# Performance work log

Measured on AMD Instinct MI355X. Metric: run time of the kernel, lower is better.

## Reference

```python
import jax, jax.numpy as jnp
import numpy as np

N = 65536          # pixels
F = 224            # spectral bands (num_features)
P = 6              # num_endmembers
H = 256            # hidden_dim


def setup_inputs() -> dict:
    key = jax.random.key(0)
    ks = jax.random.split(key, 8)
    s = lambda fan_in: 1.0 / np.sqrt(fan_in)
    return {
        "abundance_matrix": jax.random.normal(ks[0], (N, P), jnp.float32),
        "Y": jax.random.normal(ks[1], (N, F), jnp.float32),
        "W1": jax.random.normal(ks[2], (F, H), jnp.float32) * s(F),
        "b1": jnp.zeros((H,), jnp.float32),
        "W2": jax.random.normal(ks[3], (H, H), jnp.float32) * s(H),
        "b2": jnp.zeros((H,), jnp.float32),
        "W3": jax.random.normal(ks[4], (H, F), jnp.float32) * s(H),
        "b3": jnp.zeros((F,), jnp.float32),
    }


def reference(abundance_matrix, Y, W1, b1, W2, b2, W3, b3):
    # MLP is pointwise over pixels, so apply once to all pixels [N,F] -> [N,F]
    h = jax.nn.relu(Y @ W1 + b1)
    h = jax.nn.relu(h @ W2 + b2)
    logits = h @ W3 + b3                      # [N, F]

    cls = jnp.argmax(abundance_matrix, axis=-1)          # [N]
    masks = cls[None, :] == jnp.arange(P)[:, None]       # [P, N]

    # Masked per-class softmax over the pixel axis (per feature column).
    neg = jnp.finfo(logits.dtype).min
    masked_logits = jnp.where(masks[:, :, None], logits[None], neg)  # [P, N, F]
    w = jax.nn.softmax(masked_logits, axis=1)                        # [P, N, F]
    w = w * masks[:, :, None]                                        # exact zeros off-class

    M = jnp.einsum('pnf,nf->pf', w, Y)                   # [P, F] endmembers
    counts = masks.sum(axis=1)                           # [P]
    M = jnp.where((counts > 0)[:, None], M, jnp.zeros_like(M))

    Y_hat = abundance_matrix @ M                         # [N, F]
    return Y_hat
```

## Files before the change

kernel.cpp:

```cpp
#include <hip/hip_runtime.h>
#include <stdint.h>

typedef short s16x8 __attribute__((ext_vector_type(8)));
typedef short s16x4 __attribute__((ext_vector_type(4)));
typedef float f32x4 __attribute__((ext_vector_type(4)));

#define NPIX 65536
#define FEAT 224
#define PEND 6
#define HID  256

__device__ __forceinline__ unsigned short f2bf(float x) {
  unsigned u = __float_as_uint(x);
  return (unsigned short)((u + 0x7FFFu + ((u >> 16) & 1u)) >> 16);
}
__device__ __forceinline__ float bf2f(unsigned short b) {
  return __uint_as_float(((unsigned)b) << 16);
}
__device__ __forceinline__ void glds16(const void* g, void* l) {
  __builtin_amdgcn_global_load_lds(
      (const __attribute__((address_space(1))) unsigned int*)g,
      (__attribute__((address_space(3))) unsigned int*)l, 16, 0, 0);
}

__global__ void cvtW_all(const float* __restrict__ W1, const float* __restrict__ W2,
                         const float* __restrict__ W3,
                         unsigned short* __restrict__ W1t, unsigned short* __restrict__ W2t,
                         unsigned short* __restrict__ W3t, float* __restrict__ gz) {
  int i = blockIdx.x * 256 + threadIdx.x;
  if (i < 57344) {
    int n = i / 224, k = i - n * 224;
    W1t[i] = f2bf(W1[k * 256 + n]);
  } else if (i < 122880) {
    int i2 = i - 57344;
    int n = i2 >> 8, k = i2 & 255;
    W2t[i2] = f2bf(W2[k * 256 + n]);
  } else if (i < 188416) {
    int i3 = i - 122880;
    int n = i3 >> 8, k = i3 & 255;
    W3t[i3] = (n < FEAT) ? f2bf(W3[k * FEAT + n]) : (unsigned short)0;
  } else if (i < 191104) {
    gz[i - 188416] = 0.f;
  }
}

__global__ __launch_bounds__(256, 2)
void fused_mlp(const float* __restrict__ Y,
               const unsigned short* __restrict__ W1t,
               const unsigned short* __restrict__ W2t,
               const unsigned short* __restrict__ W3t,
               const float* __restrict__ b1, const float* __restrict__ b2,
               const float* __restrict__ b3, const float* __restrict__ ab,
               float* __restrict__ gsum, float* __restrict__ gsumY) {
  __shared__ __align__(16) unsigned short hS[64 * 256];
  __shared__ __align__(16) unsigned short Bs[2][8192];
  unsigned short* AsB = hS;
  float* redE = (float*)&Bs[0][0];
  float* redY = redE + PEND * FEAT;
  unsigned short* clsS = (unsigned short*)(redY + PEND * FEAT);

  const int tid = threadIdx.x;
  const int wid = tid >> 6, lane = tid & 63;
  const int wm = wid >> 1, wn = wid & 1;
  const int mrow = lane & 15, quad = lane >> 4;
  const int brow = lane >> 2, bk8 = (lane & 3) * 8;
  const int arow = tid >> 2, aqtr = tid & 3;
  const long row0 = (long)blockIdx.x * 64;

  f32x4 acc[2][8];
  float4 pv0, pv1;

#define STAGE_W(s) do {                                                     \
    const unsigned short* Wp_; int ld_, k0_;                                \
    if ((s) < 7)       { Wp_ = W1t; ld_ = 224; k0_ = (s) * 32; }            \
    else if ((s) < 15) { Wp_ = W2t; ld_ = 256; k0_ = ((s) - 7) * 32; }      \
    else               { Wp_ = W3t; ld_ = 256; k0_ = ((s) - 15) * 32; }     \
    unsigned short* dst_ = &Bs[(s) & 1][wid * 2048];                        \
    _Pragma("unroll")                                                       \
    for (int c_ = 0; c_ < 4; c_++)                                          \
      glds16(Wp_ + (wid * 64 + c_ * 16 + brow) * ld_ + k0_ + bk8,           \
             dst_ + c_ * 512);                                              \
  } while (0)

#define LOADA(p) do {                                                       \
    const float* s_ = Y + (row0 + arow) * FEAT + (p) * 32 + aqtr * 8;       \
    pv0 = *(const float4*)s_; pv1 = *(const float4*)(s_ + 4);               \
  } while (0)

#define WRITEA(p) do {                                                      \
    unsigned short* d_ = AsB + ((p) & 1) * 2304 + arow * 36 + aqtr * 8;     \
    s16x4 lo_ = {(short)f2bf(pv0.x), (short)f2bf(pv0.y),                    \
                 (short)f2bf(pv0.z), (short)f2bf(pv0.w)};                   \
    s16x4 hi_ = {(short)f2bf(pv1.x), (short)f2bf(pv1.y),                    \
                 (short)f2bf(pv1.z), (short)f2bf(pv1.w)};                   \
    *(s16x4*)d_ = lo_; *(s16x4*)(d_ + 4) = hi_;                             \
  } while (0)

#define LOAD_B(buf)                                                         \
    _Pragma("unroll")                                                       \
    for (int j = 0; j < 8; j++)                                             \
      bfv[j] = *(const s16x8*)(&Bs[buf][(wn * 128 + j * 16 + mrow) * 32 + quad * 8]);

#define MFMA_ALL()                                                          \
    _Pragma("unroll")                                                       \
    for (int i = 0; i < 2; i++)                                             \
      _Pragma("unroll")                                                     \
      for (int j = 0; j < 8; j++)                                           \
        acc[i][j] = __builtin_amdgcn_mfma_f32_16x16x32_bf16(af[i], bfv[j], acc[i][j], 0, 0, 0);

#define ZERO_ACC()                                                          \
    _Pragma("unroll")                                                       \
    for (int i = 0; i < 2; i++)                                             \
      _Pragma("unroll")                                                     \
      for (int j = 0; j < 8; j++) acc[i][j] = {0.f, 0.f, 0.f, 0.f};

  ZERO_ACC();
  LOADA(0); STAGE_W(0); WRITEA(0);
  __syncthreads();
  for (int p = 0; p < 7; p++) {
    if (p < 6) { LOADA(p + 1); STAGE_W(p + 1); }
    else       { STAGE_W(7); }
    s16x8 af[2], bfv[8];
    const unsigned short* Ab = AsB + (p & 1) * 2304;
#pragma unroll
    for (int i = 0; i < 2; i++) {
      const unsigned short* pa = Ab + (wm * 32 + i * 16 + mrow) * 36 + quad * 8;
      s16x4 lo = *(const s16x4*)pa, hi = *(const s16x4*)(pa + 4);
      af[i] = __builtin_shufflevector(lo, hi, 0, 1, 2, 3, 4, 5, 6, 7);
    }
    LOAD_B(p & 1);
    MFMA_ALL();
    if (p < 6) WRITEA(p + 1);
    __syncthreads();
  }
#pragma unroll
  for (int j = 0; j < 8; j++) {
    int col = wn * 128 + j * 16 + mrow;
    float bb = b1[col];
    int cs = col >> 3, c7 = col & 7;
#pragma unroll
    for (int i = 0; i < 2; i++) {
      int r0 = wm * 32 + i * 16 + quad * 4;
#pragma unroll
      for (int r = 0; r < 4; r++) {
        int row = r0 + r;
        hS[row * 256 + ((cs ^ (row & 7)) << 3) + c7] = f2bf(fmaxf(acc[i][j][r] + bb, 0.f));
      }
    }
  }
  __syncthreads();

  ZERO_ACC();
  for (int p = 0; p < 8; p++) {
    STAGE_W(p < 7 ? 8 + p : 15);
    const int k0 = p * 32, buf = (p + 1) & 1;
    s16x8 af[2], bfv[8];
#pragma unroll
    for (int i = 0; i < 2; i++) {
      int R = wm * 32 + i * 16 + mrow;
      int ch = (k0 >> 3) + quad;
      af[i] = *(const s16x8*)(hS + R * 256 + ((ch ^ (R & 7)) << 3));
    }
    LOAD_B(buf);
    MFMA_ALL();
    __syncthreads();
  }
#pragma unroll
  for (int j = 0; j < 8; j++) {
    int col = wn * 128 + j * 16 + mrow;
    float bb = b2[col];
    int cs = col >> 3, c7 = col & 7;
#pragma unroll
    for (int i = 0; i < 2; i++) {
      int r0 = wm * 32 + i * 16 + quad * 4;
#pragma unroll
      for (int r = 0; r < 4; r++) {
        int row = r0 + r;
        hS[row * 256 + ((cs ^ (row & 7)) << 3) + c7] = f2bf(fmaxf(acc[i][j][r] + bb, 0.f));
      }
    }
  }
  __syncthreads();

  ZERO_ACC();
  for (int p = 0; p < 8; p++) {
    if (p < 7) STAGE_W(16 + p);
    const int k0 = p * 32, buf = (p + 1) & 1;
    s16x8 af[2], bfv[8];
#pragma unroll
    for (int i = 0; i < 2; i++) {
      int R = wm * 32 + i * 16 + mrow;
      int ch = (k0 >> 3) + quad;
      af[i] = *(const s16x8*)(hS + R * 256 + ((ch ^ (R & 7)) << 3));
    }
    LOAD_B(buf);
    MFMA_ALL();
    __syncthreads();
  }
#pragma unroll
  for (int j = 0; j < 8; j++) {
    int col = wn * 128 + j * 16 + mrow;
    if (col < FEAT) {
      float bb = b3[col];
      int cs = col >> 3, c7 = col & 7;
#pragma unroll
      for (int i = 0; i < 2; i++) {
        int r0 = wm * 32 + i * 16 + quad * 4;
#pragma unroll
        for (int r = 0; r < 4; r++) {
          int row = r0 + r;
          hS[row * 256 + ((cs ^ (row & 7)) << 3) + c7] = f2bf(__expf(acc[i][j][r] + bb));
        }
      }
    }
  }
  if (tid < 64) {
    const float* a = ab + (row0 + tid) * PEND;
    float best = a[0]; int c = 0;
#pragma unroll
    for (int p = 1; p < PEND; p++) { float v = a[p]; if (v > best) { best = v; c = p; } }
    clsS[tid] = (unsigned short)c;
  }
  __syncthreads();

  const bool act = lane < 56;
  const int f0 = lane * 4;
  float accE[PEND][4], accY[PEND][4];
#pragma unroll
  for (int p = 0; p < PEND; p++)
#pragma unroll
    for (int i = 0; i < 4; i++) { accE[p][i] = 0.f; accY[p][i] = 0.f; }

#pragma unroll 4
  for (int r = wid; r < 64; r += 4) {
    int c = __builtin_amdgcn_readfirstlane((int)clsS[r]);
    if (act) {
      const unsigned short* pe = hS + r * 256 + (((f0 >> 3) ^ (r & 7)) << 3) + (f0 & 7);
      ushort4 e4 = *(const ushort4*)pe;
      float4 y4 = *(const float4*)(Y + (row0 + r) * FEAT + f0);
      float e[4] = {bf2f(e4.x), bf2f(e4.y), bf2f(e4.z), bf2f(e4.w)};
      float ey[4] = {e[0] * y4.x, e[1] * y4.y, e[2] * y4.z, e[3] * y4.w};
#define RK_CASE(P)                                                               \
      case P:                                                                    \
        _Pragma("unroll")                                                        \
        for (int i = 0; i < 4; i++) { accE[P][i] += e[i]; accY[P][i] += ey[i]; } \
        break;
      switch (c) {
        RK_CASE(0) RK_CASE(1) RK_CASE(2) RK_CASE(3) RK_CASE(4) RK_CASE(5)
      }
#undef RK_CASE
    }
  }

  for (int w = 0; w < 4; w++) {
    if (wid == w && act) {
#pragma unroll
      for (int p = 0; p < PEND; p++) {
        float4* pe = (float4*)(redE + p * FEAT + f0);
        float4* py = (float4*)(redY + p * FEAT + f0);
        float4 ve = {accE[p][0], accE[p][1], accE[p][2], accE[p][3]};
        float4 vy = {accY[p][0], accY[p][1], accY[p][2], accY[p][3]};
        if (w == 0) { *pe = ve; *py = vy; }
        else {
          float4 oe = *pe, oy = *py;
          oe.x += ve.x; oe.y += ve.y; oe.z += ve.z; oe.w += ve.w;
          oy.x += vy.x; oy.y += vy.y; oy.z += vy.z; oy.w += vy.w;
          *pe = oe; *py = oy;
        }
      }
    }
    __syncthreads();
  }

  for (int i = tid; i < PEND * FEAT; i += 256) {
    atomicAdd(&gsum[i], redE[i]);
    atomicAdd(&gsumY[i], redY[i]);
  }
#undef STAGE_W
#undef LOADA
#undef WRITEA
#undef LOAD_B
#undef MFMA_ALL
#undef ZERO_ACC
}

__global__ __launch_bounds__(256)
void yhat(const float* __restrict__ ab, const float* __restrict__ gsum,
          const float* __restrict__ gsumY, float* __restrict__ out) {
  constexpr int ROWS = 64;
  __shared__ float Ms[PEND * FEAT];
  __shared__ float aS[ROWS * PEND];
  const int tid = threadIdx.x;
  for (int i = tid; i < PEND * FEAT; i += 256) {
    float s = gsum[i];
    Ms[i] = (s > 0.f) ? gsumY[i] / s : 0.f;
  }
  const long n0 = (long)blockIdx.x * ROWS;
  for (int i = tid; i < ROWS * PEND; i += 256) aS[i] = ab[n0 * PEND + i];
  __syncthreads();

  const int wid = tid >> 6;
  const int lane = tid & 63;
  if (lane >= 56) return;
  const int f0 = lane * 4;
  float4 Mr[PEND];
#pragma unroll
  for (int p = 0; p < PEND; p++) Mr[p] = *(const float4*)(Ms + p * FEAT + f0);

  for (int r = wid; r < ROWS; r += 4) {
    float a[PEND];
#pragma unroll
    for (int p = 0; p < PEND; p++) a[p] = aS[r * PEND + p];
    float4 o = {0.f, 0.f, 0.f, 0.f};
#pragma unroll
    for (int p = 0; p < PEND; p++) {
      o.x += a[p] * Mr[p].x; o.y += a[p] * Mr[p].y;
      o.z += a[p] * Mr[p].z; o.w += a[p] * Mr[p].w;
    }
    *(float4*)(out + (n0 + r) * FEAT + f0) = o;
  }
}

extern "C" void kernel_launch(void* const* d_in, const int* in_sizes, int n_in,
                              void* d_out, int out_size, void* d_ws, size_t ws_size,
                              hipStream_t stream) {
  const float* ab = (const float*)d_in[0];
  const float* Y  = (const float*)d_in[1];
  const float* W1 = (const float*)d_in[2];
  const float* b1 = (const float*)d_in[3];
  const float* W2 = (const float*)d_in[4];
  const float* b2 = (const float*)d_in[5];
  const float* W3 = (const float*)d_in[6];
  const float* b3 = (const float*)d_in[7];
  float* out = (float*)d_out;

  char* ws = (char*)d_ws;
  const size_t oW1t  = 0;
  const size_t oW2t  = 114688;
  const size_t oW3t  = 245760;
  const size_t osum  = 376832;

  unsigned short* W1t = (unsigned short*)(ws + oW1t);
  unsigned short* W2t = (unsigned short*)(ws + oW2t);
  unsigned short* W3t = (unsigned short*)(ws + oW3t);
  float* gsum  = (float*)(ws + osum);
  float* gsumY = (float*)(ws + osum + 5376);

  cvtW_all<<<747, 256, 0, stream>>>(W1, W2, W3, W1t, W2t, W3t, gsum);
  fused_mlp<<<1024, 256, 0, stream>>>(Y, W1t, W2t, W3t, b1, b2, b3, ab, gsum, gsumY);
  yhat<<<1024, 256, 0, stream>>>(ab, gsum, gsumY, out);
}
```

Measured before the change: 203.9 us.

## Give each wave its own output columns and drop per-step barriers in layers 2-3

The wave tiling changes from a 2x2 grid (32 rows x 128 cols per wave) to a 1x4 grid (all 64 rows x 64 cols per wave). Each wave now reads only the weight rows it staged itself into LDS, so the per-k-step __syncthreads in the second and third GEMM loops become explicit vmcnt waits, and the remaining barriers use lgkmcnt(0)+s_barrier. MFMA sections are also wrapped in s_setprio raises. This aims to cut barrier stalls and let waves run out of step, at the cost of relying on hand-written waitcnt correctness for the async global-to-LDS double buffer.

Result: no change. 201.1 us (-1.4%).

```diff
diff --git a/kernel.cpp b/kernel.cpp
--- a/kernel.cpp
+++ b/kernel.cpp
@@ -22,6 +22,9 @@
       (const __attribute__((address_space(1))) unsigned int*)g,
       (__attribute__((address_space(3))) unsigned int*)l, 16, 0, 0);
 }
+
+#define WAITV(n) asm volatile("s_waitcnt vmcnt(" #n ")" ::: "memory")
+#define BAR_LGKM() asm volatile("s_waitcnt lgkmcnt(0)\ns_barrier" ::: "memory")
 
 __global__ void cvtW_all(const float* __restrict__ W1, const float* __restrict__ W2,
                          const float* __restrict__ W3,
@@ -61,13 +64,12 @@
 
   const int tid = threadIdx.x;
   const int wid = tid >> 6, lane = tid & 63;
-  const int wm = wid >> 1, wn = wid & 1;
   const int mrow = lane & 15, quad = lane >> 4;
   const int brow = lane >> 2, bk8 = (lane & 3) * 8;
   const int arow = tid >> 2, aqtr = tid & 3;
   const long row0 = (long)blockIdx.x * 64;
 
-  f32x4 acc[2][8];
+  f32x4 acc[4][4];
   float4 pv0, pv1;
 
 #define STAGE_W(s) do {                                                     \
@@ -98,117 +100,120 @@
 
 #define LOAD_B(buf)                                                         \
     _Pragma("unroll")                                                       \
-    for (int j = 0; j < 8; j++)                                             \
-      bfv[j] = *(const s16x8*)(&Bs[buf][(wn * 128 + j * 16 + mrow) * 32 + quad * 8]);
-
-#define MFMA_ALL()                                                          \
+    for (int j = 0; j < 4; j++)                                             \
+      bfv[j] = *(const s16x8*)(&Bs[buf][(wid * 64 + j * 16 + mrow) * 32 + quad * 8]);
+
+#define MFMA_ALL() do {                                                     \
+    __builtin_amdgcn_s_setprio(1);                                          \
     _Pragma("unroll")                                                       \
-    for (int i = 0; i < 2; i++)                                             \
+    for (int i = 0; i < 4; i++)                                             \
       _Pragma("unroll")                                                     \
-      for (int j = 0; j < 8; j++)                                           \
-        acc[i][j] = __builtin_amdgcn_mfma_f32_16x16x32_bf16(af[i], bfv[j], acc[i][j], 0, 0, 0);
+      for (int j = 0; j < 4; j++)                                           \
+        acc[i][j] = __builtin_amdgcn_mfma_f32_16x16x32_bf16(af[i], bfv[j], acc[i][j], 0, 0, 0); \
+    __builtin_amdgcn_s_setprio(0);                                          \
+  } while (0)
 
 #define ZERO_ACC()                                                          \
     _Pragma("unroll")                                                       \
-    for (int i = 0; i < 2; i++)                                             \
+    for (int i = 0; i < 4; i++)                                             \
       _Pragma("unroll")                                                     \
-      for (int j = 0; j < 8; j++) acc[i][j] = {0.f, 0.f, 0.f, 0.f};
+      for (int j = 0; j < 4; j++) acc[i][j] = {0.f, 0.f, 0.f, 0.f};
 
   ZERO_ACC();
   LOADA(0); STAGE_W(0); WRITEA(0);
   __syncthreads();
   for (int p = 0; p < 7; p++) {
-    if (p < 6) { LOADA(p + 1); STAGE_W(p + 1); }
-    else       { STAGE_W(7); }
-    s16x8 af[2], bfv[8];
+    if (p < 6) { LOADA(p + 1); STAGE_W(p + 1); WAITV(6); }
+    else       { STAGE_W(7);   WAITV(4); }
+    s16x8 af[4], bfv[4];
     const unsigned short* Ab = AsB + (p & 1) * 2304;
 #pragma unroll
-    for (int i = 0; i < 2; i++) {
-      const unsigned short* pa = Ab + (wm * 32 + i * 16 + mrow) * 36 + quad * 8;
+    for (int i = 0; i < 4; i++) {
+      const unsigned short* pa = Ab + (i * 16 + mrow) * 36 + quad * 8;
       s16x4 lo = *(const s16x4*)pa, hi = *(const s16x4*)(pa + 4);
       af[i] = __builtin_shufflevector(lo, hi, 0, 1, 2, 3, 4, 5, 6, 7);
     }
     LOAD_B(p & 1);
     MFMA_ALL();
     if (p < 6) WRITEA(p + 1);
-    __syncthreads();
-  }
-#pragma unroll
-  for (int j = 0; j < 8; j++) {
-    int col = wn * 128 + j * 16 + mrow;
+    BAR_LGKM();
+  }
+#pragma unroll
+  for (int j = 0; j < 4; j++) {
+    int col = wid * 64 + j * 16 + mrow;
     float bb = b1[col];
     int cs = col >> 3, c7 = col & 7;
 #pragma unroll
-    for (int i = 0; i < 2; i++) {
-      int r0 = wm * 32 + i * 16 + quad * 4;
+    for (int i = 0; i < 4; i++) {
 #pragma unroll
       for (int r = 0; r < 4; r++) {
-        int row = r0 + r;
+        int row = i * 16 + quad * 4 + r;
         hS[row * 256 + ((cs ^ (row & 7)) << 3) + c7] = f2bf(fmaxf(acc[i][j][r] + bb, 0.f));
       }
     }
   }
-  __syncthreads();
+  BAR_LGKM();
 
   ZERO_ACC();
   for (int p = 0; p < 8; p++) {
-    STAGE_W(p < 7 ? 8 + p : 15);
-    const int k0 = p * 32, buf = (p + 1) & 1;
-    s16x8 af[2], bfv[8];
-#pragma unroll
-    for (int i = 0; i < 2; i++) {
-      int R = wm * 32 + i * 16 + mrow;
+    STAGE_W(8 + p);
+    WAITV(4);
+    const int k0 = p * 32;
+    s16x8 af[4], bfv[4];
+#pragma unroll
+    for (int i = 0; i < 4; i++) {
+      int R = i * 16 + mrow;
       int ch = (k0 >> 3) + quad;
       af[i] = *(const s16x8*)(hS + R * 256 + ((ch ^ (R & 7)) << 3));
     }
-    LOAD_B(buf);
+    LOAD_B((7 + p) & 1);
     MFMA_ALL();
-    __syncthreads();
-  }
-#pragma unroll
-  for (int j = 0; j < 8; j++) {
-    int col = wn * 128 + j * 16 + mrow;
+  }
+  BAR_LGKM();
+#pragma unroll
+  for (int j = 0; j < 4; j++) {
+    int col = wid * 64 + j * 16 + mrow;
     float bb = b2[col];
     int cs = col >> 3, c7 = col & 7;
 #pragma unroll
-    for (int i = 0; i < 2; i++) {
-      int r0 = wm * 32 + i * 16 + quad * 4;
+    for (int i = 0; i < 4; i++) {
 #pragma unroll
       for (int r = 0; r < 4; r++) {
-        int row = r0 + r;
+        int row = i * 16 + quad * 4 + r;
         hS[row * 256 + ((cs ^ (row & 7)) << 3) + c7] = f2bf(fmaxf(acc[i][j][r] + bb, 0.f));
       }
     }
   }
-  __syncthreads();
+  BAR_LGKM();
 
   ZERO_ACC();
   for (int p = 0; p < 8; p++) {
-    if (p < 7) STAGE_W(16 + p);
-    const int k0 = p * 32, buf = (p + 1) & 1;
-    s16x8 af[2], bfv[8];
-#pragma unroll
-    for (int i = 0; i < 2; i++) {
-      int R = wm * 32 + i * 16 + mrow;
+    if (p < 7) { STAGE_W(16 + p); WAITV(4); }
+    else       { WAITV(0); }
+    const int k0 = p * 32;
+    s16x8 af[4], bfv[4];
+#pragma unroll
+    for (int i = 0; i < 4; i++) {
+      int R = i * 16 + mrow;
       int ch = (k0 >> 3) + quad;
       af[i] = *(const s16x8*)(hS + R * 256 + ((ch ^ (R & 7)) << 3));
     }
-    LOAD_B(buf);
+    LOAD_B((15 + p) & 1);
     MFMA_ALL();
-    __syncthreads();
-  }
-#pragma unroll
-  for (int j = 0; j < 8; j++) {
-    int col = wn * 128 + j * 16 + mrow;
+  }
+  BAR_LGKM();
+
+#pragma unroll
+  for (int j = 0; j < 4; j++) {
+    int col = wid * 64 + j * 16 + mrow;
     if (col < FEAT) {
       float bb = b3[col];
       int cs = col >> 3, c7 = col & 7;
 #pragma unroll
-      for (int i = 0; i < 2; i++) {
-        int r0 = wm * 32 + i * 16 + quad * 4;
+      for (int i = 0; i < 4; i++) {
 #pragma unroll
         for (int r = 0; r < 4; r++) {
-          int row = r0 + r;
+          int row = i * 16 + quad * 4 + r;
           hS[row * 256 + ((cs ^ (row & 7)) << 3) + c7] = f2bf(__expf(acc[i][j][r] + bb));
         }
       }
@@ -221,7 +226,7 @@
     for (int p = 1; p < PEND; p++) { float v = a[p]; if (v > best) { best = v; c = p; } }
     clsS[tid] = (unsigned short)c;
   }
-  __syncthreads();
+  BAR_LGKM();
 
   const bool act = lane < 56;
   const int f0 = lane * 4;
```
